# Kernel optimization log

Measured on AMD Instinct MI355X. Metric: run time of the kernel, lower is better.

## Reference

```python
import jax, jax.numpy as jnp
import numpy as np

N, H, W, C = 8, 64, 64, 256
GC = 8            # channels per group (gc)
G = C // GC       # groups = 32
K = 3             # deformable kernel size
KK = K * K
DK = 3            # depthwise kernel size for offset/mask branch


def setup_inputs() -> dict:
    key = jax.random.key(0)
    ks = jax.random.split(key, 6)
    s = 0.02
    return {
        "x": jax.random.normal(ks[0], (N, H, W, C), jnp.float32),
        "dw_w": jax.random.normal(ks[1], (DK, DK, 1, C), jnp.float32) * s,
        "dw_b": jnp.zeros((C,), jnp.float32),
        "om_w": jax.random.normal(ks[2], (C, G * KK * 3), jnp.float32) * s,
        "om_b": jnp.zeros((G * KK * 3,), jnp.float32),
        "vp_w": jax.random.normal(ks[3], (C, C), jnp.float32) * s,
        "vp_b": jnp.zeros((C,), jnp.float32),
        "op_w": jax.random.normal(ks[4], (C, C), jnp.float32) * s,  # output_bias=False
    }


def _dcnv4(x, dw_w, dw_b, om_w, om_b, vp_w, vp_b, op_w):
    n, h, w, c = x.shape
    # --- offset/mask branch: depthwise conv then pointwise linear ---
    xdw = jax.lax.conv_general_dilated(
        x, dw_w, window_strides=(1, 1), padding="SAME",
        dimension_numbers=("NHWC", "HWIO", "NHWC"), feature_group_count=c) + dw_b
    om = (xdw @ om_w + om_b).reshape(n, h, w, G, KK * 3)
    offset = om[..., : 2 * KK].reshape(n, h, w, G, KK, 2)  # (dx, dy) per point
    mask = om[..., 2 * KK :]                                # [n,h,w,G,KK], raw (no softmax in v4)

    # --- value projection ---
    value = (x @ vp_w + vp_b).reshape(n, h, w, G, GC)

    # --- sampling locations: pixel + kernel-grid point + learned offset ---
    kg = (jnp.arange(K) - (K - 1) // 2).astype(jnp.float32)
    ky = jnp.repeat(kg, K)   # [KK]
    kx = jnp.tile(kg, K)     # [KK]
    base_y = jnp.arange(h, dtype=jnp.float32).reshape(1, h, 1, 1, 1)
    base_x = jnp.arange(w, dtype=jnp.float32).reshape(1, 1, w, 1, 1)
    py = base_y + ky + offset[..., 1]  # [n,h,w,G,KK]
    px = base_x + kx + offset[..., 0]

    y0 = jnp.floor(py)
    x0 = jnp.floor(px)
    ty = py - y0
    tx = px - x0

    n_idx = jnp.arange(n).reshape(n, 1, 1, 1, 1)
    g_idx = jnp.arange(G).reshape(1, 1, 1, G, 1)

    def gather(yi, xi):
        valid = (yi >= 0) & (yi <= h - 1) & (xi >= 0) & (xi <= w - 1)
        yc = jnp.clip(yi, 0, h - 1).astype(jnp.int32)
        xc = jnp.clip(xi, 0, w - 1).astype(jnp.int32)
        v = value[n_idx, yc, xc, g_idx]          # [n,h,w,G,KK,GC]
        return v * valid[..., None].astype(value.dtype)

    v00 = gather(y0, x0)
    v01 = gather(y0, x0 + 1)
    v10 = gather(y0 + 1, x0)
    v11 = gather(y0 + 1, x0 + 1)

    sampled = ((1 - ty) * (1 - tx))[..., None] * v00 \
            + ((1 - ty) * tx)[..., None] * v01 \
            + (ty * (1 - tx))[..., None] * v10 \
            + (ty * tx)[..., None] * v11        # [n,h,w,G,KK,GC]

    out = jnp.einsum("nhwgkc,nhwgk->nhwgc", sampled, mask).reshape(n, h, w, c)
    return out @ op_w                            # output proj, no bias


def reference(x, dw_w, dw_b, om_w, om_b, vp_w, vp_b, op_w):
    return _dcnv4(x, dw_w, dw_b, om_w, om_b, vp_w, vp_b, op_w)
```

## Files before the change

### kernel.cpp

```cpp
#include <hip/hip_runtime.h>


typedef __bf16 bf16_t;
typedef bf16_t bf16x8 __attribute__((ext_vector_type(8)));
typedef bf16_t bf16x4 __attribute__((ext_vector_type(4)));
typedef float f32x4 __attribute__((ext_vector_type(4)));

namespace {
constexpr int NN = 8, HH = 64, WW = 64, CC = 256;
constexpr int G = 32, GC = 8, OMD = 864;
constexpr int NPIX = NN * HH * WW;
constexpr int OMD_PAD = 896;
}

__device__ __forceinline__ size_t fragIdx(int row, int c) {
  return ((size_t)(row >> 4) * 4096) + ((c >> 5) * 512) + (((c >> 3) & 3) * 128) +
         ((row & 15) * 8) + (c & 7);
}

__global__ __launch_bounds__(256) void convert_weights_kernel(
    const float* __restrict__ om_w, const float* __restrict__ vp_w,
    const float* __restrict__ op_w, bf16_t* __restrict__ om_wF,
    bf16_t* __restrict__ vp_wF, bf16_t* __restrict__ op_wF) {
  __shared__ float s_t[64][65];
  const int b = blockIdx.x, t = threadIdx.x;
  const float* src;
  bf16_t* dst;
  int ld, ncols, nt, kt;
  if (b < 56) {
    src = om_w; dst = om_wF; ld = OMD; ncols = OMD; kt = b / 14; nt = b % 14;
  } else if (b < 72) {
    const int i = b - 56;
    src = vp_w; dst = vp_wF; ld = CC; ncols = CC; kt = i >> 2; nt = i & 3;
  } else {
    const int i = b - 72;
    src = op_w; dst = op_wF; ld = CC; ncols = CC; kt = i >> 2; nt = i & 3;
  }
  const int nl = t & 63, kh = t >> 6;
  const int n = nt * 64 + nl;
#pragma unroll
  for (int i = 0; i < 16; ++i) {
    const int kl = kh * 16 + i;
    s_t[kl][nl] = (n < ncols) ? src[(size_t)(kt * 64 + kl) * ld + n] : 0.0f;
  }
  __syncthreads();
  const int lane = t & 63, kq = lane >> 4, n15 = lane & 15, n16 = t >> 6;
#pragma unroll
  for (int it = 0; it < 2; ++it) {
    bf16x8 v;
#pragma unroll
    for (int j = 0; j < 8; ++j) v[j] = (bf16_t)s_t[it * 32 + kq * 8 + j][n16 * 16 + n15];
    const size_t off = (size_t)(nt * 4 + n16) * 4096 + (size_t)(kt * 2 + it) * 512 +
                       kq * 128 + n15 * 8;
    *(bf16x8*)(dst + off) = v;
  }
}

__global__ __launch_bounds__(256) void dwconv_row_kernel(
    const float* __restrict__ x, const float* __restrict__ dw_w,
    const float* __restrict__ dw_b, bf16_t* __restrict__ xdwF,
    bf16_t* __restrict__ x_bf16F) {
  const int t = threadIdx.x;
  const int cq = (t & 63) * 4;
  const int seg = t >> 6;
  const int row = blockIdx.x >> 1;
  const int half = blockIdx.x & 1;
  const int y = row & 63;
  const bool up = (y > 0), dn = (y < HH - 1);
  const float* xrow = x + (size_t)row * WW * CC + cq;

  const float4 bias = *(const float4*)&dw_b[cq];
  float4 dw[9];
#pragma unroll
  for (int i = 0; i < 9; ++i) dw[i] = *(const float4*)&dw_w[(size_t)i * CC + cq];

  const float4 zero = make_float4(0.f, 0.f, 0.f, 0.f);
  auto loadcol = [&](int xx, float4 c[3]) {
    if (xx < 0 || xx >= WW) { c[0] = c[1] = c[2] = zero; return; }
    c[0] = up ? *(const float4*)(xrow + ((size_t)xx - WW) * CC) : zero;
    c[1] = *(const float4*)(xrow + (size_t)xx * CC);
    c[2] = dn ? *(const float4*)(xrow + ((size_t)xx + WW) * CC) : zero;
  };

  const int x0 = half * 32 + seg * 8;
  float4 cm[3], cc[3], cp[3];
  loadcol(x0 - 1, cm);
  loadcol(x0, cc);

  for (int xx = x0; xx < x0 + 8; ++xx) {
    loadcol(xx + 1, cp);
    float4 a = bias;
#pragma unroll
    for (int r = 0; r < 3; ++r) {
      const float4 w0 = dw[r * 3 + 0], w1 = dw[r * 3 + 1], w2 = dw[r * 3 + 2];
      a.x = fmaf(cm[r].x, w0.x, fmaf(cc[r].x, w1.x, fmaf(cp[r].x, w2.x, a.x)));
      a.y = fmaf(cm[r].y, w0.y, fmaf(cc[r].y, w1.y, fmaf(cp[r].y, w2.y, a.y)));
      a.z = fmaf(cm[r].z, w0.z, fmaf(cc[r].z, w1.z, fmaf(cp[r].z, w2.z, a.z)));
      a.w = fmaf(cm[r].w, w0.w, fmaf(cc[r].w, w1.w, fmaf(cp[r].w, w2.w, a.w)));
    }
    const int pix = row * WW + xx;
    const size_t o = fragIdx(pix, cq);
    bf16x4 av, cv;
    av[0] = (bf16_t)a.x; av[1] = (bf16_t)a.y; av[2] = (bf16_t)a.z; av[3] = (bf16_t)a.w;
    cv[0] = (bf16_t)cc[1].x; cv[1] = (bf16_t)cc[1].y;
    cv[2] = (bf16_t)cc[1].z; cv[3] = (bf16_t)cc[1].w;
    *(bf16x4*)&xdwF[o] = av;
    *(bf16x4*)&x_bf16F[o] = cv;
#pragma unroll
    for (int r = 0; r < 3; ++r) { cm[r] = cc[r]; cc[r] = cp[r]; }
  }
}

template <bool HAS_BIAS, int OUTMODE>
__global__ __launch_bounds__(512, 4) void mfma_gemm256_kernel(
    const bf16_t* __restrict__ AF, const bf16_t* __restrict__ BF,
    const float* __restrict__ bias, void* __restrict__ outp) {
  __shared__ bf16_t s_val[OUTMODE == 1 ? 64 : 1][OUTMODE == 1 ? 264 : 1];
  const int lane = threadIdx.x & 63;
  const int wave = threadIdx.x >> 6;
  const int mq = wave >> 1;
  const int nh = wave & 1;
  const int mt = blockIdx.x * 4 + mq;
  const int m = lane & 15;
  const int kq = lane >> 4;

  const bf16_t* Ap = AF + (size_t)mt * 4096 + lane * 8;
  const bf16_t* Bp = BF + (size_t)(nh * 8) * 4096 + lane * 8;

  f32x4 acc[8] = {};
#pragma unroll
  for (int ks = 0; ks < 8; ++ks) {
    const bf16x8 a = *(const bf16x8*)(Ap + ks * 512);
#pragma unroll
    for (int i = 0; i < 8; ++i) {
      const bf16x8 b = *(const bf16x8*)(Bp + (size_t)i * 4096 + ks * 512);
      acc[i] = __builtin_amdgcn_mfma_f32_16x16x32_bf16(a, b, acc[i], 0, 0, 0);
    }
  }

#pragma unroll
  for (int i = 0; i < 8; ++i) {
    const int n = (nh * 8 + i) * 16 + m;
    const float bs = HAS_BIAS ? bias[n] : 0.0f;
#pragma unroll
    for (int r = 0; r < 4; ++r) {
      const float v = acc[i][r] + bs;
      if (OUTMODE == 0) {
        const int pix = mt * 16 + kq * 4 + r;
        ((float*)outp)[(size_t)pix * CC + n] = v;
      } else {
        const int pl = mq * 16 + kq * 4 + r;
        s_val[pl][n] = (bf16_t)v;
      }
    }
  }

  if (OUTMODE == 1) {
    __syncthreads();
    const int p16 = lane & 15;
    const int gl = lane >> 4;
    const int pt = wave & 3;
    const int gh = wave >> 2;
    const int pl = pt * 16 + p16;
    const int pixg = blockIdx.x * 64 + pl;
    const int img = pixg >> 12;
    bf16_t* vg = (bf16_t*)outp;
#pragma unroll
    for (int i = 0; i < 4; ++i) {
      const int g = i * 8 + gh * 4 + gl;
      const bf16x8 v = *(const bf16x8*)&s_val[pl][g * 8];
      *(bf16x8*)(vg + ((size_t)(img * G + g) << 15) + (size_t)(pixg & 4095) * GC) = v;
    }
  }
}

__global__ __launch_bounds__(512, 4) void om_sample_mfma_kernel(
    const bf16_t* __restrict__ xdwF, const bf16_t* __restrict__ om_wF,
    const float* __restrict__ om_b, const bf16_t* __restrict__ value_g,
    bf16_t* __restrict__ sampledF) {
  constexpr int GS = 32;
  __shared__ bf16_t s_om[32][1024];

  const int lane = threadIdx.x & 63;
  const int wave = threadIdx.x >> 6;
  const int pix0 = blockIdx.x * 32;

  {
    const int m = lane & 15;
    const int kq = lane >> 4;
    const bf16_t* Ap = xdwF + (size_t)(blockIdx.x * 2) * 4096 + lane * 8;
    const bf16_t* Bp = om_wF + (size_t)(wave * 7) * 4096 + lane * 8;
    f32x4 acc[2][7] = {};
#pragma unroll
    for (int ks = 0; ks < 8; ++ks) {
      const bf16x8 a0 = *(const bf16x8*)(Ap + ks * 512);
      const bf16x8 a1 = *(const bf16x8*)(Ap + 4096 + ks * 512);
#pragma unroll
      for (int i = 0; i < 7; ++i) {
        const bf16x8 b = *(const bf16x8*)(Bp + (size_t)i * 4096 + ks * 512);
        acc[0][i] = __builtin_amdgcn_mfma_f32_16x16x32_bf16(a0, b, acc[0][i], 0, 0, 0);
        acc[1][i] = __builtin_amdgcn_mfma_f32_16x16x32_bf16(a1, b, acc[1][i], 0, 0, 0);
      }
    }
#pragma unroll
    for (int i = 0; i < 7; ++i) {
      const int nt = wave * 7 + i;
      if (nt < 54) {
        const int n = nt * 16 + m;
        const float bs = om_b[n];
        const int g = n / 27;
        const int j = n - 27 * g;
#pragma unroll
        for (int mt2 = 0; mt2 < 2; ++mt2)
#pragma unroll
          for (int r = 0; r < 4; ++r)
            s_om[mt2 * 16 + kq * 4 + r][g * GS + j] = (bf16_t)(acc[mt2][i][r] + bs);
      }
    }
  }
  __syncthreads();

  const int gl = lane >> 4;
  const int g = wave * 4 + gl;
#pragma unroll
  for (int iter = 0; iter < 2; ++iter) {
    const int p = (lane & 15) + iter * 16;
    const int pix = pix0 + p;
    const int xw = pix & 63;
    const int y = (pix >> 6) & 63;
    const int img = pix >> 12;
    const bf16_t* plane = value_g + ((size_t)(img * G + g) << 15);

    const bf16_t* omp = &s_om[p][g * GS];
    const bf16x8 o0 = *(const bf16x8*)(omp);
    const bf16x8 o1 = *(const bf16x8*)(omp + 8);
    const bf16x8 o2 = *(const bf16x8*)(omp + 16);
    const bf16x8 o3 = *(const bf16x8*)(omp + 24);
    float arr[27];
#pragma unroll
    for (int j = 0; j < 8; ++j) {
      arr[j] = (float)o0[j];
      arr[8 + j] = (float)o1[j];
      arr[16 + j] = (float)o2[j];
    }
#pragma unroll
    for (int j = 0; j < 3; ++j) arr[24 + j] = (float)o3[j];

    float acc[GC];
#pragma unroll
    for (int c = 0; c < GC; ++c) acc[c] = 0.0f;

#pragma unroll
    for (int k = 0; k < 9; ++k) {
      const float px = (float)(xw + (k % 3) - 1) + arr[2 * k];
      const float py = (float)(y + (k / 3) - 1) + arr[2 * k + 1];
      const float mk = arr[18 + k];
      const float x0f = floorf(px), y0f = floorf(py);
      const float tx = px - x0f, ty = py - y0f;
      const int ix = (int)x0f, iy = (int)y0f;

      const float vx0 = (ix >= 0 && ix < WW) ? 1.0f : 0.0f;
      const float vx1 = (ix + 1 >= 0 && ix + 1 < WW) ? 1.0f : 0.0f;
      const float vy0 = (iy >= 0 && iy < HH) ? 1.0f : 0.0f;
      const float vy1 = (iy + 1 >= 0 && iy + 1 < HH) ? 1.0f : 0.0f;
      const int ix0 = min(max(ix, 0), WW - 1);
      const int ix1 = min(max(ix + 1, 0), WW - 1);
      const int iy0 = min(max(iy, 0), HH - 1);
      const int iy1 = min(max(iy + 1, 0), HH - 1);

      const bf16x8 v00 = *(const bf16x8*)(plane + (size_t)(iy0 * WW + ix0) * GC);
      const bf16x8 v01 = *(const bf16x8*)(plane + (size_t)(iy0 * WW + ix1) * GC);
      const bf16x8 v10 = *(const bf16x8*)(plane + (size_t)(iy1 * WW + ix0) * GC);
      const bf16x8 v11 = *(const bf16x8*)(plane + (size_t)(iy1 * WW + ix1) * GC);

      const float w00 = mk * (1.0f - ty) * (1.0f - tx) * vy0 * vx0;
      const float w01 = mk * (1.0f - ty) * tx * vy0 * vx1;
      const float w10 = mk * ty * (1.0f - tx) * vy1 * vx0;
      const float w11 = mk * ty * tx * vy1 * vx1;

#pragma unroll
      for (int c = 0; c < GC; ++c) {
        float s = acc[c];
        s = fmaf(w00, (float)v00[c], s);
        s = fmaf(w01, (float)v01[c], s);
        s = fmaf(w10, (float)v10[c], s);
        s = fmaf(w11, (float)v11[c], s);
        acc[c] = s;
      }
    }

    bf16x8 sv;
#pragma unroll
    for (int c = 0; c < GC; ++c) sv[c] = (bf16_t)acc[c];
    *(bf16x8*)(sampledF + (size_t)(blockIdx.x * 2 + iter) * 4096 + wave * 512 +
               lane * 8) = sv;
  }
}

extern "C" void kernel_launch(void* const* d_in, const int* in_sizes, int n_in,
                              void* d_out, int out_size, void* d_ws, size_t ws_size,
                              hipStream_t stream) {
  const float* x = (const float*)d_in[0];
  const float* dw_w = (const float*)d_in[1];
  const float* dw_b = (const float*)d_in[2];
  const float* om_w = (const float*)d_in[3];
  const float* om_b = (const float*)d_in[4];
  const float* vp_w = (const float*)d_in[5];
  const float* vp_b = (const float*)d_in[6];
  const float* op_w = (const float*)d_in[7];
  float* out = (float*)d_out;

  char* ws = (char*)d_ws;
  bf16_t* value_g = (bf16_t*)ws;
  bf16_t* xdwF = (bf16_t*)(ws + 16777216);
  bf16_t* x_bf16F = (bf16_t*)(ws + 33554432);
  bf16_t* sampledF = x_bf16F;
  bf16_t* om_wF = (bf16_t*)(ws + 50331648);
  bf16_t* vp_wF = (bf16_t*)(ws + 50790400);
  bf16_t* op_wF = (bf16_t*)(ws + 50921472);

  convert_weights_kernel<<<88, 256, 0, stream>>>(om_w, vp_w, op_w,
                                                 om_wF, vp_wF, op_wF);
  dwconv_row_kernel<<<NN * HH * 2, 256, 0, stream>>>(x, dw_w, dw_b, xdwF, x_bf16F);
  mfma_gemm256_kernel<true, 1><<<NPIX / 64, 512, 0, stream>>>(x_bf16F, vp_wF, vp_b, value_g);
  om_sample_mfma_kernel<<<NPIX / 32, 512, 0, stream>>>(xdwF, om_wF, om_b, value_g, sampledF);
  mfma_gemm256_kernel<false, 0><<<NPIX / 64, 512, 0, stream>>>(sampledF, op_wF, nullptr, out);
}
```

Measured before the change: 230.5 us.

## Fuse depthwise conv with value projection GEMM and swizzle offset smem layout

Merges the depthwise conv kernel and the value-projection MFMA GEMM into one kernel per image row. The bf16 copy of x stays in shared memory, so it is no longer written to and reread from global memory, and one launch disappears. The om_sample kernel's shared-memory offset/mask buffer now uses a rotated (swizzled) layout to avoid bank conflicts. The trade-offs: the fused kernel writes value_g as scattered 2-byte stores instead of staging them for vectorized stores, and its block count halves to one block per row.

```diff
diff --git a/kernel.cpp b/kernel.cpp
--- a/kernel.cpp
+++ b/kernel.cpp
@@ -10,7 +10,6 @@
 constexpr int NN = 8, HH = 64, WW = 64, CC = 256;
 constexpr int G = 32, GC = 8, OMD = 864;
 constexpr int NPIX = NN * HH * WW;
-constexpr int OMD_PAD = 896;
 }
 
 __device__ __forceinline__ size_t fragIdx(int row, int c) {
@@ -56,120 +55,102 @@
   }
 }
 
-__global__ __launch_bounds__(256) void dwconv_row_kernel(
+__global__ __launch_bounds__(512, 4) void dwconv_value_kernel(
     const float* __restrict__ x, const float* __restrict__ dw_w,
-    const float* __restrict__ dw_b, bf16_t* __restrict__ xdwF,
-    bf16_t* __restrict__ x_bf16F) {
+    const float* __restrict__ dw_b, const bf16_t* __restrict__ vp_wF,
+    const float* __restrict__ vp_b, bf16_t* __restrict__ xdwF,
+    bf16_t* __restrict__ value_g) {
+  __shared__ bf16_t s_xf[64 * 256];
+
   const int t = threadIdx.x;
-  const int cq = (t & 63) * 4;
-  const int seg = t >> 6;
-  const int row = blockIdx.x >> 1;
-  const int half = blockIdx.x & 1;
+  const int row = blockIdx.x;
   const int y = row & 63;
-  const bool up = (y > 0), dn = (y < HH - 1);
-  const float* xrow = x + (size_t)row * WW * CC + cq;
-
-  const float4 bias = *(const float4*)&dw_b[cq];
-  float4 dw[9];
-#pragma unroll
-  for (int i = 0; i < 9; ++i) dw[i] = *(const float4*)&dw_w[(size_t)i * CC + cq];
-
-  const float4 zero = make_float4(0.f, 0.f, 0.f, 0.f);
-  auto loadcol = [&](int xx, float4 c[3]) {
-    if (xx < 0 || xx >= WW) { c[0] = c[1] = c[2] = zero; return; }
-    c[0] = up ? *(const float4*)(xrow + ((size_t)xx - WW) * CC) : zero;
-    c[1] = *(const float4*)(xrow + (size_t)xx * CC);
-    c[2] = dn ? *(const float4*)(xrow + ((size_t)xx + WW) * CC) : zero;
-  };
-
-  const int x0 = half * 32 + seg * 8;
-  float4 cm[3], cc[3], cp[3];
-  loadcol(x0 - 1, cm);
-  loadcol(x0, cc);
-
-  for (int xx = x0; xx < x0 + 8; ++xx) {
-    loadcol(xx + 1, cp);
-    float4 a = bias;
-#pragma unroll
-    for (int r = 0; r < 3; ++r) {
-      const float4 w0 = dw[r * 3 + 0], w1 = dw[r * 3 + 1], w2 = dw[r * 3 + 2];
-      a.x = fmaf(cm[r].x, w0.x, fmaf(cc[r].x, w1.x, fmaf(cp[r].x, w2.x, a.x)));
-      a.y = fmaf(cm[r].y, w0.y, fmaf(cc[r].y, w1.y, fmaf(cp[r].y, w2.y, a.y)));
-      a.z = fmaf(cm[r].z, w0.z, fmaf(cc[r].z, w1.z, fmaf(cp[r].z, w2.z, a.z)));
-      a.w = fmaf(cm[r].w, w0.w, fmaf(cc[r].w, w1.w, fmaf(cp[r].w, w2.w, a.w)));
-    }
-    const int pix = row * WW + xx;
-    const size_t o = fragIdx(pix, cq);
-    bf16x4 av, cv;
-    av[0] = (bf16_t)a.x; av[1] = (bf16_t)a.y; av[2] = (bf16_t)a.z; av[3] = (bf16_t)a.w;
-    cv[0] = (bf16_t)cc[1].x; cv[1] = (bf16_t)cc[1].y;
-    cv[2] = (bf16_t)cc[1].z; cv[3] = (bf16_t)cc[1].w;
-    *(bf16x4*)&xdwF[o] = av;
-    *(bf16x4*)&x_bf16F[o] = cv;
-#pragma unroll
-    for (int r = 0; r < 3; ++r) { cm[r] = cc[r]; cc[r] = cp[r]; }
-  }
-}
-
-template <bool HAS_BIAS, int OUTMODE>
-__global__ __launch_bounds__(512, 4) void mfma_gemm256_kernel(
-    const bf16_t* __restrict__ AF, const bf16_t* __restrict__ BF,
-    const float* __restrict__ bias, void* __restrict__ outp) {
-  __shared__ bf16_t s_val[OUTMODE == 1 ? 64 : 1][OUTMODE == 1 ? 264 : 1];
-  const int lane = threadIdx.x & 63;
-  const int wave = threadIdx.x >> 6;
-  const int mq = wave >> 1;
-  const int nh = wave & 1;
-  const int mt = blockIdx.x * 4 + mq;
-  const int m = lane & 15;
-  const int kq = lane >> 4;
-
-  const bf16_t* Ap = AF + (size_t)mt * 4096 + lane * 8;
-  const bf16_t* Bp = BF + (size_t)(nh * 8) * 4096 + lane * 8;
-
-  f32x4 acc[8] = {};
-#pragma unroll
-  for (int ks = 0; ks < 8; ++ks) {
-    const bf16x8 a = *(const bf16x8*)(Ap + ks * 512);
+  const int img = row >> 6;
+
+  {
+    const int cq = (t & 63) * 4;
+    const int seg = t >> 6;
+    const bool up = (y > 0), dn = (y < HH - 1);
+    const float* xrow = x + (size_t)row * WW * CC + cq;
+
+    const float4 bias = *(const float4*)&dw_b[cq];
+    float4 dw[9];
+#pragma unroll
+    for (int i = 0; i < 9; ++i) dw[i] = *(const float4*)&dw_w[(size_t)i * CC + cq];
+
+    const float4 zero = make_float4(0.f, 0.f, 0.f, 0.f);
+    auto loadcol = [&](int xx, float4 c[3]) {
+      if (xx < 0 || xx >= WW) { c[0] = c[1] = c[2] = zero; return; }
+      c[0] = up ? *(const float4*)(xrow + ((size_t)xx - WW) * CC) : zero;
+      c[1] = *(const float4*)(xrow + (size_t)xx * CC);
+      c[2] = dn ? *(const float4*)(xrow + ((size_t)xx + WW) * CC) : zero;
+    };
+
+    const int x0 = seg * 8;
+    float4 cm[3], cc[3], cp[3];
+    loadcol(x0 - 1, cm);
+    loadcol(x0, cc);
+
+    for (int xx = x0; xx < x0 + 8; ++xx) {
+      loadcol(xx + 1, cp);
+      float4 a = bias;
+#pragma unroll
+      for (int r = 0; r < 3; ++r) {
+        const float4 w0 = dw[r * 3 + 0], w1 = dw[r * 3 + 1], w2 = dw[r * 3 + 2];
+        a.x = fmaf(cm[r].x, w0.x, fmaf(cc[r].x, w1.x, fmaf(cp[r].x, w2.x, a.x)));
+        a.y = fmaf(cm[r].y, w0.y, fmaf(cc[r].y, w1.y, fmaf(cp[r].y, w2.y, a.y)));
+        a.z = fmaf(cm[r].z, w0.z, fmaf(cc[r].z, w1.z, fmaf(cp[r].z, w2.z, a.z)));
+        a.w = fmaf(cm[r].w, w0.w, fmaf(cc[r].w, w1.w, fmaf(cp[r].w, w2.w, a.w)));
+      }
+      const int pix = row * WW + xx;
+      bf16x4 av, cv;
+      av[0] = (bf16_t)a.x; av[1] = (bf16_t)a.y; av[2] = (bf16_t)a.z; av[3] = (bf16_t)a.w;
+      cv[0] = (bf16_t)cc[1].x; cv[1] = (bf16_t)cc[1].y;
+      cv[2] = (bf16_t)cc[1].z; cv[3] = (bf16_t)cc[1].w;
+      *(bf16x4*)&xdwF[fragIdx(pix, cq)] = av;
+      const int lf = (xx >> 4) * 4096 + ((cq >> 5) * 512) + (((cq >> 3) & 3) * 128) +
+                     ((xx & 15) * 8) + (cq & 7);
+      *(bf16x4*)&s_xf[lf] = cv;
+#pragma unroll
+      for (int r = 0; r < 3; ++r) { cm[r] = cc[r]; cc[r] = cp[r]; }
+    }
+  }
+  __syncthreads();
+
+  {
+    const int lane = t & 63;
+    const int wave = t >> 6;
+    const int mq = wave >> 1;
+    const int nh = wave & 1;
+    const int m = lane & 15;
+    const int kq = lane >> 4;
+
+    const bf16_t* Ap = s_xf + mq * 4096 + lane * 8;
+    const bf16_t* Bp = vp_wF + (size_t)(nh * 8) * 4096 + lane * 8;
+
+    f32x4 acc[8] = {};
+#pragma unroll
+    for (int ks = 0; ks < 8; ++ks) {
+      const bf16x8 a = *(const bf16x8*)(Ap + ks * 512);
+#pragma unroll
+      for (int i = 0; i < 8; ++i) {
+        const bf16x8 b = *(const bf16x8*)(Bp + (size_t)i * 4096 + ks * 512);
+        acc[i] = __builtin_amdgcn_mfma_f32_16x16x32_bf16(a, b, acc[i], 0, 0, 0);
+      }
+    }
+
 #pragma unroll
     for (int i = 0; i < 8; ++i) {
-      const bf16x8 b = *(const bf16x8*)(Bp + (size_t)i * 4096 + ks * 512);
-      acc[i] = __builtin_amdgcn_mfma_f32_16x16x32_bf16(a, b, acc[i], 0, 0, 0);
-    }
-  }
-
-#pragma unroll
-  for (int i = 0; i < 8; ++i) {
-    const int n = (nh * 8 + i) * 16 + m;
-    const float bs = HAS_BIAS ? bias[n] : 0.0f;
-#pragma unroll
-    for (int r = 0; r < 4; ++r) {
-      const float v = acc[i][r] + bs;
-      if (OUTMODE == 0) {
-        const int pix = mt * 16 + kq * 4 + r;
-        ((float*)outp)[(size_t)pix * CC + n] = v;
-      } else {
+      const int n = (nh * 8 + i) * 16 + m;
+      const float bs = vp_b[n];
+      const int g = n >> 3, c = n & 7;
+      bf16_t* plane = value_g + ((size_t)(img * G + g) << 15) + c;
+#pragma unroll
+      for (int r = 0; r < 4; ++r) {
         const int pl = mq * 16 + kq * 4 + r;
-        s_val[pl][n] = (bf16_t)v;
-      }
-    }
-  }
-
-  if (OUTMODE == 1) {
-    __syncthreads();
-    const int p16 = lane & 15;
-    const int gl = lane >> 4;
-    const int pt = wave & 3;
-    const int gh = wave >> 2;
-    const int pl = pt * 16 + p16;
-    const int pixg = blockIdx.x * 64 + pl;
-    const int img = pixg >> 12;
-    bf16_t* vg = (bf16_t*)outp;
-#pragma unroll
-    for (int i = 0; i < 4; ++i) {
-      const int g = i * 8 + gh * 4 + gl;
-      const bf16x8 v = *(const bf16x8*)&s_val[pl][g * 8];
-      *(bf16x8*)(vg + ((size_t)(img * G + g) << 15) + (size_t)(pixg & 4095) * GC) = v;
+        const int pin = y * 64 + pl;
+        plane[(size_t)pin * GC] = (bf16_t)(acc[i][r] + bs);
+      }
     }
   }
 }
@@ -178,8 +159,7 @@
     const bf16_t* __restrict__ xdwF, const bf16_t* __restrict__ om_wF,
     const float* __restrict__ om_b, const bf16_t* __restrict__ value_g,
     bf16_t* __restrict__ sampledF) {
-  constexpr int GS = 32;
-  __shared__ bf16_t s_om[32][1024];
+  __shared__ bf16_t s_om[32 * 1024];
 
   const int lane = threadIdx.x & 63;
   const int wave = threadIdx.x >> 6;
@@ -210,11 +190,15 @@
         const float bs = om_b[n];
         const int g = n / 27;
         const int j = n - 27 * g;
+        const int cj = j >> 3, jl = j & 7;
 #pragma unroll
         for (int mt2 = 0; mt2 < 2; ++mt2)
 #pragma unroll
-          for (int r = 0; r < 4; ++r)
-            s_om[mt2 * 16 + kq * 4 + r][g * GS + j] = (bf16_t)(acc[mt2][i][r] + bs);
+          for (int r = 0; r < 4; ++r) {
+            const int p = mt2 * 16 + kq * 4 + r;
+            s_om[p * 1024 + (((g * 4 + cj + p) & 127) * 8) + jl] =
+                (bf16_t)(acc[mt2][i][r] + bs);
+          }
       }
     }
   }
@@ -231,11 +215,12 @@
     const int img = pix >> 12;
     const bf16_t* plane = value_g + ((size_t)(img * G + g) << 15);
 
-    const bf16_t* omp = &s_om[p][g * GS];
-    const bf16x8 o0 = *(const bf16x8*)(omp);
-    const bf16x8 o1 = *(const bf16x8*)(omp + 8);
-    const bf16x8 o2 = *(const bf16x8*)(omp + 16);
-    const bf16x8 o3 = *(const bf16x8*)(omp + 24);
+    const bf16_t* omp = &s_om[p * 1024];
+    const int g4p = g * 4 + p;
+    const bf16x8 o0 = *(const bf16x8*)(omp + ((g4p + 0) & 127) * 8);
+    const bf16x8 o1 = *(const bf16x8*)(omp + ((g4p + 1) & 127) * 8);
+    const bf16x8 o2 = *(const bf16x8*)(omp + ((g4p + 2) & 127) * 8);
+    const bf16x8 o3 = *(const bf16x8*)(omp + ((g4p + 3) & 127) * 8);
     float arr[27];
 #pragma unroll
     for (int j = 0; j < 8; ++j) {
@@ -294,6 +279,42 @@
     for (int c = 0; c < GC; ++c) sv[c] = (bf16_t)acc[c];
     *(bf16x8*)(sampledF + (size_t)(blockIdx.x * 2 + iter) * 4096 + wave * 512 +
                lane * 8) = sv;
+  }
+}
+
+__global__ __launch_bounds__(512, 4) void out_gemm_kernel(
+    const bf16_t* __restrict__ AF, const bf16_t* __restrict__ BF,
+    float* __restrict__ out) {
+  const int lane = threadIdx.x & 63;
+  const int wave = threadIdx.x >> 6;
+  const int mq = wave >> 1;
+  const int nh = wave & 1;
+  const int mt = blockIdx.x * 4 + mq;
+  const int m = lane & 15;
+  const int kq = lane >> 4;
+
+  const bf16_t* Ap = AF + (size_t)mt * 4096 + lane * 8;
+  const bf16_t* Bp = BF + (size_t)(nh * 8) * 4096 + lane * 8;
+
+  f32x4 acc[8] = {};
+#pragma unroll
+  for (int ks = 0; ks < 8; ++ks) {
+    const bf16x8 a = *(const bf16x8*)(Ap + ks * 512);
+#pragma unroll
+    for (int i = 0; i < 8; ++i) {
+      const bf16x8 b = *(const bf16x8*)(Bp + (size_t)i * 4096 + ks * 512);
+      acc[i] = __builtin_amdgcn_mfma_f32_16x16x32_bf16(a, b, acc[i], 0, 0, 0);
+    }
+  }
+
+#pragma unroll
+  for (int i = 0; i < 8; ++i) {
+    const int n = (nh * 8 + i) * 16 + m;
+#pragma unroll
+    for (int r = 0; r < 4; ++r) {
+      const int pix = mt * 16 + kq * 4 + r;
+      out[(size_t)pix * CC + n] = acc[i][r];
+    }
   }
 }
 
@@ -313,16 +334,16 @@
   char* ws = (char*)d_ws;
   bf16_t* value_g = (bf16_t*)ws;
   bf16_t* xdwF = (bf16_t*)(ws + 16777216);
-  bf16_t* x_bf16F = (bf16_t*)(ws + 33554432);
-  bf16_t* sampledF = x_bf16F;
+  bf16_t* sampledF = (bf16_t*)(ws + 33554432);
   bf16_t* om_wF = (bf16_t*)(ws + 50331648);
   bf16_t* vp_wF = (bf16_t*)(ws + 50790400);
   bf16_t* op_wF = (bf16_t*)(ws + 50921472);
 
   convert_weights_kernel<<<88, 256, 0, stream>>>(om_w, vp_w, op_w,
                                                  om_wF, vp_wF, op_wF);
-  dwconv_row_kernel<<<NN * HH * 2, 256, 0, stream>>>(x, dw_w, dw_b, xdwF, x_bf16F);
-  mfma_gemm256_kernel<true, 1><<<NPIX / 64, 512, 0, stream>>>(x_bf16F, vp_wF, vp_b, value_g);
-  om_sample_mfma_kernel<<<NPIX / 32, 512, 0, stream>>>(xdwF, om_wF, om_b, value_g, sampledF);
-  mfma_gemm256_kernel<false, 0><<<NPIX / 64, 512, 0, stream>>>(sampledF, op_wF, nullptr, out);
-}
+  dwconv_value_kernel<<<NN * HH, 512, 0, stream>>>(x, dw_w, dw_b, vp_wF, vp_b,
+                                                   xdwF, value_g);
+  om_sample_mfma_kernel<<<NPIX / 32, 512, 0, stream>>>(xdwF, om_wF, om_b,
+                                                       value_g, sampledF);
+  out_gemm_kernel<<<NPIX / 64, 512, 0, stream>>>(sampledF, op_wF, out);
+}
```

Measured after the change: 212.1 us. -8.0%, faster.
